# Optimization experiments

Hardware: AMD Instinct MI355X
Metric: run time of the kernel (lower is better)

The kernel has to match this reference:

```python
import jax, jax.numpy as jnp
import numpy as np

N = 1048576        # number of raw proposals
NC = 2             # num classes (source hardcodes self.nc = 2)
CONF_THRES = 0.25  # score_thres
IOU_THRES = 0.45
MAX_WH = 4096.0    # class offset for class-aware NMS (agnostic=False)
MAX_NMS = 30000    # cap on boxes entering NMS
MAX_DET = 300      # cap on detections returned


def setup_inputs() -> dict:
    key = jax.random.key(0)
    k1, k2, k3, k4 = jax.random.split(key, 4)
    xy = jax.random.uniform(k1, (1, N, 2), dtype=jnp.float32) * 640.0          # box centers (pixels)
    wh = jax.random.uniform(k2, (1, N, 2), dtype=jnp.float32) * 98.0 + 2.0     # widths/heights in [2, 100]
    obj = jax.random.uniform(k3, (1, N, 1), dtype=jnp.float32)                 # objectness
    cls = jax.random.uniform(k4, (1, N, NC), dtype=jnp.float32)                # class scores
    prediction = jnp.concatenate([xy, wh, obj, cls], axis=-1)                  # [1, N, 4+1+nc]
    return {"prediction": prediction}


def reference(prediction):
    # Single image (source only ever fills/returns output[0]).
    pred = prediction[0]                        # [N, 7]
    obj = pred[:, 4]                            # objectness
    cls = pred[:, 5:5 + NC] * obj[:, None]      # conf = obj * cls  (nc > 1 branch)
    conf = jnp.max(cls, axis=-1)                # best-class confidence
    j = jnp.argmax(cls, axis=-1)                # best-class index

    # xywh -> xyxy
    xy, wh = pred[:, :2], pred[:, 2:4]
    box = jnp.concatenate([xy - wh * 0.5, xy + wh * 0.5], axis=-1)  # [N, 4]

    # candidate mask: obj > thres (xc) AND best-class conf > thres
    valid = (obj > CONF_THRES) & (conf > CONF_THRES)
    scores = jnp.where(valid, conf, -1.0)

    # n > max_nms: keep top MAX_NMS by confidence (argsort descending truncation)
    top_s, top_i = jax.lax.top_k(scores, MAX_NMS)       # [MAX_NMS]
    box_t = box[top_i]                                   # [MAX_NMS, 4]
    conf_t = conf[top_i]
    j_t = j[top_i]

    # class-aware NMS: offset boxes per class so classes never suppress each other
    boxes_off = box_t + (j_t.astype(box_t.dtype) * MAX_WH)[:, None]
    area = (boxes_off[:, 2] - boxes_off[:, 0]) * (boxes_off[:, 3] - boxes_off[:, 1])

    # Greedy NMS: iteratively select max-score box, suppress IoU > thres.
    # Selecting the argmax each step is equivalent to sorted greedy NMS, and
    # MAX_DET steps yields exactly the first max_det kept indices.
    def step(s, _):
        idx = jnp.argmax(s)
        ok = s[idx] > 0.0                       # any real candidate left?
        b = boxes_off[idx]
        lt = jnp.maximum(b[:2], boxes_off[:, :2])
        rb = jnp.minimum(b[2:], boxes_off[:, 2:])
        inter = jnp.prod(jnp.clip(rb - lt, 0.0), axis=-1)
        iou = inter / (area[idx] + area - inter)
        s = jnp.where(ok & (iou > IOU_THRES), -1.0, s)  # suppress (incl. self, IoU=1)
        return s, (idx, ok)

    _, (sel, ok) = jax.lax.scan(step, top_s, None, length=MAX_DET)

    dets = jnp.concatenate(
        [box_t[sel], conf_t[sel, None], j_t[sel, None].astype(box_t.dtype)], axis=-1
    )                                           # [MAX_DET, 6] = [xyxy, conf, cls]
    dets = dets * ok[:, None].astype(dets.dtype)  # zero out padding rows
    return dets, ok
```

## Files before the change

kernel.cpp:

```cpp
#include <hip/hip_runtime.h>
#include <stdint.h>

#pragma clang fp contract(off)

#define N_ELEM   1048576
#define MAX_NMS  30000
#define MAX_DET  300
#define IOU_T    0.45f
#define CONF_T   0.25f
#define SOA_N    30720
#define KMIN     0xBE800000u
#define EQCAP    2048
#define RPW      16

typedef uint32_t u32;
typedef unsigned long long u64;

#define C_CB   0
#define C_KP   1
#define C_A    2
#define C_NUM  3
#define C_EQC  4

__device__ inline u32 monokey(float s){
  u32 b = __float_as_uint(s);
  return b ^ ((b & 0x80000000u) ? 0xFFFFFFFFu : 0x80000000u);
}
__device__ inline int binOf(u32 k){
  u32 d = (k - KMIN) >> 8;
  return d > 65535u ? 65535 : (int)d;
}
__device__ inline u64 shfl64(u64 v, int src){
  int lo = __shfl((int)(u32)(v & 0xFFFFFFFFull), src);
  int hi = __shfl((int)(u32)(v >> 32), src);
  return ((u64)(u32)hi << 32) | (u32)lo;
}

__global__ void kkeys(const float4* __restrict__ pred4, u32* __restrict__ keys,
                      u32* __restrict__ hist){
  __shared__ float lds[1792];
  int t = threadIdx.x;
  const float4* src = pred4 + (size_t)blockIdx.x * 448;
  float4* l4 = (float4*)lds;
  #pragma unroll
  for (int k = 0; k < 2; k++){
    int idx = k*256 + t;
    if (idx < 448) l4[idx] = src[idx];
  }
  __syncthreads();
  float obj = lds[t*7 + 4], c0 = lds[t*7 + 5], c1 = lds[t*7 + 6];
  float p0 = c0*obj, p1 = c1*obj;
  float conf = fmaxf(p0, p1);
  bool valid = (obj > CONF_T) && (conf > CONF_T);
  float score = valid ? conf : -1.0f;
  u32 mk = monokey(score);
  keys[blockIdx.x*256 + t] = mk;
  if (mk > KMIN) atomicAdd(&hist[binOf(mk)], 1u);
}

__global__ void __launch_bounds__(1024) kselect(const u32* __restrict__ hist,
                                                u32* __restrict__ binBase,
                                                u32* __restrict__ ctrl){
  __shared__ u32 csum[1024];
  __shared__ u32 s[1024];
  __shared__ int selC;
  __shared__ u32 chunk[64];
  int t = threadIdx.x, lane = t & 63, wv = t >> 6;
  for (int j = 0; j < 64; j++){
    int c = wv*64 + j;
    u32 v = hist[c*64 + lane];
    #pragma unroll
    for (int off = 32; off > 0; off >>= 1) v += __shfl_down(v, off);
    if (lane == 0) csum[c] = v;
  }
  __syncthreads();
  u32 own = csum[t];
  s[t] = own; __syncthreads();
  for (int off = 1; off < 1024; off <<= 1){
    u32 v = s[t];
    u32 add = (t + off < 1024) ? s[t + off] : 0u;
    __syncthreads();
    s[t] = v + add;
    __syncthreads();
  }
  u32 above = s[t] - own;
  u32 grand = s[0];
  csum[t] = above;
  const u32 K = MAX_NMS;
  if (grand >= K && above < K && K <= above + own){ selC = t; }
  __syncthreads();
  if (grand >= K && t < 64) chunk[t] = hist[selC*64 + t];
  __syncthreads();
  if (t == 0){
    if (grand < K){
      ctrl[C_CB] = 0xFFFFFFFFu; ctrl[C_KP] = 0; ctrl[C_A] = grand; ctrl[C_NUM] = grand;
    } else {
      u32 cum = csum[selC];
      for (int b = 63; b >= 0; b--){
        u32 c = chunk[b];
        if (cum + c >= K){
          ctrl[C_CB] = (u32)(selC*64 + b);
          ctrl[C_KP] = K - cum;
          ctrl[C_A]  = cum;
          ctrl[C_NUM] = K;
          break;
        }
        cum += c;
      }
    }
  }
  for (int j = 0; j < 64; j++){
    int c = wv*64 + j;
    u32 v = hist[c*64 + lane];
    u32 suf = v;
    #pragma unroll
    for (int off = 1; off < 64; off <<= 1){
      u32 o = __shfl_down(suf, off);
      suf += (lane + off < 64) ? o : 0u;
    }
    binBase[c*64 + lane] = csum[c] + suf - v;
  }
}

__global__ void kscatter(const uint4* __restrict__ keys4, const u32* __restrict__ binBase,
                         u32* __restrict__ binCursor, u32* __restrict__ ctrl,
                         u32* __restrict__ binnedKey, u32* __restrict__ binnedIdx,
                         u32* __restrict__ eqKey, u32* __restrict__ eqIdx){
  int t = blockIdx.x*blockDim.x + threadIdx.x;
  if (t >= N_ELEM/4) return;
  int cb = (int)ctrl[C_CB];
  uint4 kv = keys4[t];
  u32 kk[4] = {kv.x, kv.y, kv.z, kv.w};
  #pragma unroll
  for (int r = 0; r < 4; r++){
    u32 k = kk[r];
    if (k <= KMIN) continue;
    int b = binOf(k);
    u32 i = (u32)(t*4 + r);
    if (b > cb){
      u32 pos = binBase[b] + atomicAdd(&binCursor[b], 1u);
      if (pos < MAX_NMS){ binnedKey[pos] = k; binnedIdx[pos] = i; }
    } else if (b == cb){
      u32 e = atomicAdd(&ctrl[C_EQC], 1u);
      if (e < EQCAP){ eqKey[e] = k; eqIdx[e] = i; }
    }
  }
}

__device__ inline void writeSoA(const float* __restrict__ pred, float* __restrict__ soa,
                                u32 r, u32 i){
  const float* row = pred + (size_t)i*7;
  float x = row[0], y = row[1], w = row[2], hh = row[3];
  float obj = row[4], c0 = row[5], c1 = row[6];
  float p0 = c0*obj, p1 = c1*obj;
  float conf = fmaxf(p0, p1);
  float jf = (p0 >= p1) ? 0.0f : 1.0f;
  float bx1 = x - w*0.5f, by1 = y - hh*0.5f;
  float bx2 = x + w*0.5f, by2 = y + hh*0.5f;
  float off = jf * 4096.0f;
  float ox1 = bx1 + off, oy1 = by1 + off, ox2 = bx2 + off, oy2 = by2 + off;
  float area = (ox2 - ox1) * (oy2 - oy1);
  soa[r + 0*SOA_N] = ox1;  soa[r + 1*SOA_N] = oy1;
  soa[r + 2*SOA_N] = ox2;  soa[r + 3*SOA_N] = oy2;
  soa[r + 4*SOA_N] = area; soa[r + 5*SOA_N] = conf;
  soa[r + 6*SOA_N] = jf;
  soa[r + 7*SOA_N] = bx1;  soa[r + 8*SOA_N] = by1;
  soa[r + 9*SOA_N] = bx2;  soa[r +10*SOA_N] = by2;
}

__global__ void krank(const float* __restrict__ pred, const u32* __restrict__ binnedKey,
                      const u32* __restrict__ binnedIdx, const u32* __restrict__ binBase,
                      const u32* __restrict__ binHist, const u32* __restrict__ ctrl,
                      const u32* __restrict__ eqKey, const u32* __restrict__ eqIdx,
                      float* __restrict__ soa){
  int p = blockIdx.x*blockDim.x + threadIdx.x;
  u32 A = ctrl[C_A], Kp = ctrl[C_KP];
  if (Kp > 0){
    u32 n = ctrl[C_EQC]; if (n > EQCAP) n = EQCAP;
    if (p < (int)n){
      u32 k = eqKey[p], i = eqIdx[p];
      u32 r = 0;
      for (u32 m = 0; m < n; m++){
        u32 km = eqKey[m], im = eqIdx[m];
        r += (km > k) || (km == k && im < i);
      }
      if (r < Kp) writeSoA(pred, soa, A + r, i);
    }
  }
  if (p < (int)A){
    u32 k = binnedKey[p]; u32 i = binnedIdx[p];
    if (i >= N_ELEM) i = 0;
    int b = binOf(k);
    u32 st = binBase[b], cnt = binHist[b];
    u32 r = st;
    for (u32 q = st; q < st + cnt; q++){
      u32 kq = binnedKey[q], iq = binnedIdx[q];
      if (kq > k || (kq == k && iq < i)) r++;
    }
    if (r < A) writeSoA(pred, soa, r, i);
  }
}

__global__ void kmask(const float* __restrict__ soa, u64* __restrict__ mask,
                      int W, int WBsh, int nUnits){
  int lane = threadIdx.x & 63;
  int gw = (blockIdx.x*blockDim.x + threadIdx.x) >> 6;
  int nwaves = (gridDim.x*blockDim.x) >> 6;
  int WB = 1 << WBsh;
  for (int u = gw; u < nUnits; u += nwaves){
    int rowg = u >> WBsh;
    int w = u & (WB - 1);
    if (((w + 1) << 6) <= rowg*RPW) continue;
    int j = (w << 6) + lane;
    float cx1 = soa[j], cy1 = soa[j + SOA_N], cx2 = soa[j + 2*SOA_N],
          cy2 = soa[j + 3*SOA_N], ca = soa[j + 4*SOA_N];
    #pragma unroll
    for (int rr = 0; rr < RPW; rr++){
      int i = rowg*RPW + rr;
      if (w < (i >> 6)) continue;
      float rx1 = soa[i], ry1 = soa[i + SOA_N], rx2 = soa[i + 2*SOA_N],
            ry2 = soa[i + 3*SOA_N], ra = soa[i + 4*SOA_N];
      float ltx = fmaxf(rx1, cx1), lty = fmaxf(ry1, cy1);
      float rbx = fminf(rx2, cx2), rby = fminf(ry2, cy2);
      float iw = fmaxf(rbx - ltx, 0.0f), ih = fmaxf(rby - lty, 0.0f);
      float inter = iw * ih;
      float iou = inter / ((ra + ca) - inter);
      u64 m = __ballot(iou > IOU_T);
      if (lane == 0) mask[(size_t)i*WB + w] = m;
    }
  }
}

__global__ void __launch_bounds__(64) kwalk(const float* __restrict__ soa,
                                            const u64* __restrict__ mask,
                                            const u32* __restrict__ ctrl,
                                            float* __restrict__ out, int out_size,
                                            int W){
  __shared__ float kx1[320], ky1[320], kx2[320], ky2[320], ka[320];
  __shared__ u64 dlds[64];
  int lane = threadIdx.x;
  for (int o = lane; o < out_size; o += 64) out[o] = 0.0f;
  int numCand = (int)ctrl[C_NUM];
  int WB = W >> 6;
  int lim = numCand < W ? numCand : W;
  int nb = (lim + 63) >> 6;
  u64 rem0 = 0, rem1 = 0;
  int nsel = 0;

  u64 diag = 0;
  if (nb > 0 && lane < lim) diag = mask[(size_t)lane*WB + 0];

  for (int bi = 0; bi < nb && nsel < MAX_DET; bi++){
    u64 remw = (bi < 64) ? shfl64(rem0, bi) : shfl64(rem1, bi - 64);
    u64 w = ~remw;
    int rb = lim - (bi << 6);
    if (rb < 64) w &= ((1ull << rb) - 1ull);
    dlds[lane] = diag;
    __syncthreads();

    u64 diagn = 0;
    int inext = (bi + 1)*64 + lane;
    if (bi + 1 < nb && inext < lim) diagn = mask[(size_t)inext*WB + (bi + 1)];

    u64 sel = 0;
    int room = MAX_DET - nsel;
    while (w){
      int b = (int)__builtin_ctzll(w);
      sel |= (1ull << b);
      if (--room == 0) break;
      u64 rw = dlds[b];
      w &= ~rw;
      w &= ~(1ull << b);
    }
    int cnt = __popcll(sel);

    u64 s = sel;
    long long ids[8];
    #pragma unroll
    for (int q = 0; q < 8; q++){
      if (s){ ids[q] = (long long)((bi << 6) + __builtin_ctzll(s)); s &= s - 1; }
      else ids[q] = -1;
    }
    u64 a0[8], a1[8];
    #pragma unroll
    for (int q = 0; q < 8; q++){
      a0[q] = 0; a1[q] = 0;
      if (ids[q] >= 0){
        const u64* rp = mask + (size_t)ids[q]*WB;
        if (lane < WB)      a0[q] = rp[lane];
        if (64 + lane < WB) a1[q] = rp[64 + lane];
      }
    }

    if (lane < cnt){
      u64 t = sel;
      for (int q = 0; q < lane; q++) t &= t - 1;
      int b = (int)__builtin_ctzll(t);
      int i = (bi << 6) + b;
      int r = nsel + lane;
      kx1[r] = soa[i];            ky1[r] = soa[i + SOA_N];
      kx2[r] = soa[i + 2*SOA_N];  ky2[r] = soa[i + 3*SOA_N];
      ka[r]  = soa[i + 4*SOA_N];
      float* dr = out + r*6;
      dr[0] = soa[i + 7*SOA_N];  dr[1] = soa[i + 8*SOA_N];
      dr[2] = soa[i + 9*SOA_N];  dr[3] = soa[i + 10*SOA_N];
      dr[4] = soa[i + 5*SOA_N];  dr[5] = soa[i + 6*SOA_N];
      out[MAX_DET*6 + r] = 1.0f;
    }
    nsel += cnt;

    #pragma unroll
    for (int q = 0; q < 8; q++){ rem0 |= a0[q]; rem1 |= a1[q]; }

    while (s){
      long long ids2[8];
      #pragma unroll
      for (int q = 0; q < 8; q++){
        if (s){ ids2[q] = (long long)((bi << 6) + __builtin_ctzll(s)); s &= s - 1; }
        else ids2[q] = -1;
      }
      u64 b0[8], b1[8];
      #pragma unroll
      for (int q = 0; q < 8; q++){
        b0[q] = 0; b1[q] = 0;
        if (ids2[q] >= 0){
          const u64* rp = mask + (size_t)ids2[q]*WB;
          if (lane < WB)      b0[q] = rp[lane];
          if (64 + lane < WB) b1[q] = rp[64 + lane];
        }
      }
      #pragma unroll
      for (int q = 0; q < 8; q++){ rem0 |= b0[q]; rem1 |= b1[q]; }
    }
    diag = diagn;
    __syncthreads();
  }

  if (nsel < MAX_DET && numCand > W){
    for (int base = W; base < numCand && nsel < MAX_DET; base += 64){
      int li = base + lane;
      bool has = li < numCand;
      float cox1=0.f,coy1=0.f,cox2=0.f,coy2=0.f,car=1.f,csc=-1.f,ccl=0.f;
      float cbx1=0.f,cby1=0.f,cbx2=0.f,cby2=0.f;
      if (has){
        cox1 = soa[li]; coy1 = soa[li + SOA_N]; cox2 = soa[li + 2*SOA_N];
        coy2 = soa[li + 3*SOA_N]; car = soa[li + 4*SOA_N];
        csc = soa[li + 5*SOA_N]; ccl = soa[li + 6*SOA_N];
        cbx1 = soa[li + 7*SOA_N]; cby1 = soa[li + 8*SOA_N];
        cbx2 = soa[li + 9*SOA_N]; cby2 = soa[li + 10*SOA_N];
      }
      int m = min(64, numCand - base);
      for (int t2 = 0; t2 < m && nsel < MAX_DET; t2++){
        float qx1 = __shfl(cox1, t2), qy1 = __shfl(coy1, t2);
        float qx2 = __shfl(cox2, t2), qy2 = __shfl(coy2, t2);
        float qa  = __shfl(car,  t2);
        bool supp = false;
        #pragma unroll
        for (int q = 0; q < 5; q++){
          int slot = lane + (q << 6);
          if (slot < nsel){
            float ltx = fmaxf(qx1, kx1[slot]), lty = fmaxf(qy1, ky1[slot]);
            float rbx = fminf(qx2, kx2[slot]), rby = fminf(qy2, ky2[slot]);
            float iw = fmaxf(rbx - ltx, 0.0f), ih = fmaxf(rby - lty, 0.0f);
            float inter = iw * ih;
            float iou = inter / ((qa + ka[slot]) - inter);
            supp = supp || (iou > IOU_T);
          }
        }
        if (__any(supp)) continue;
        float bx1 = __shfl(cbx1, t2), by1 = __shfl(cby1, t2);
        float bx2 = __shfl(cbx2, t2), by2 = __shfl(cby2, t2);
        float sc  = __shfl(csc,  t2), cl  = __shfl(ccl,  t2);
        if (lane == 0){
          kx1[nsel] = qx1; ky1[nsel] = qy1; kx2[nsel] = qx2; ky2[nsel] = qy2; ka[nsel] = qa;
          float* dr = out + nsel*6;
          dr[0] = bx1; dr[1] = by1; dr[2] = bx2; dr[3] = by2; dr[4] = sc; dr[5] = cl;
          out[MAX_DET*6 + nsel] = 1.0f;
        }
        nsel++;
      }
    }
  }
}

extern "C" void kernel_launch(void* const* d_in, const int* in_sizes, int n_in,
                              void* d_out, int out_size, void* d_ws, size_t ws_size,
                              hipStream_t stream){
  const float* pred = (const float*)d_in[0];
  float* out = (float*)d_out;
  char* w = (char*)d_ws;

  u32*  keys       = (u32*)(w + 0x000000);
  u32*  hist       = (u32*)(w + 0x400000);
  u32*  binCursor  = (u32*)(w + 0x440000);
  u32*  ctrl       = (u32*)(w + 0x480000);
  u32*  binBase    = (u32*)(w + 0x4C0000);
  u32*  eqKey      = (u32*)(w + 0x500000);
  u32*  eqIdx      = (u32*)(w + 0x502000);
  u32*  binnedKey  = (u32*)(w + 0x510000);
  u32*  binnedIdx  = (u32*)(w + 0x530000);
  float* soa       = (float*)(w + 0x550000);
  u64*  mask       = (u64*)(w + 0x6A0000);

  int W, WBsh;
  if      (ws_size >= 0xEA0000){ W = 8192; WBsh = 7; }
  else if (ws_size >= 0x8A0000){ W = 4096; WBsh = 6; }
  else                         { W = 2048; WBsh = 5; }

  hipMemsetAsync(hist, 0, 0x80100, stream);

  kkeys   <<<4096, 256, 0, stream>>>((const float4*)pred, keys, hist);
  kselect <<<1, 1024, 0, stream>>>(hist, binBase, ctrl);
  kscatter<<<1024, 256, 0, stream>>>((const uint4*)keys, binBase, binCursor, ctrl,
                                     binnedKey, binnedIdx, eqKey, eqIdx);
  krank   <<<(MAX_NMS + 255)/256 + 1, 256, 0, stream>>>(pred, binnedKey, binnedIdx, binBase,
                                                        hist, ctrl, eqKey, eqIdx, soa);
  int nUnits = (W/RPW) << WBsh;
  kmask   <<<2048, 256, 0, stream>>>(soa, mask, W, WBsh, nUnits);
  kwalk   <<<1, 64, 0, stream>>>(soa, mask, ctrl, out, out_size, W);
}
```

Before: 325.3 us.

## Fuse selection pipeline into one cooperative kernel with grid syncs

Merges the histogram, threshold selection, scatter, rank and mask-building stages into a single cooperative kernel of 512 blocks separated by grid-wide barriers, replacing five launches plus a memset. The single-block selection step is spread across blocks: each block computes chunk sums in parallel and redundantly does the 256-wide scan. The aim is to remove launch gaps and the serial single-block selection kernel. In exchange, the grid barriers add overhead, and the rank and mask stages now run on a smaller fixed grid with occupancy capped by launch bounds.

```diff
diff --git a/kernel.cpp b/kernel.cpp
--- a/kernel.cpp
+++ b/kernel.cpp
@@ -1,7 +1,10 @@
 #include <hip/hip_runtime.h>
+#include <hip/hip_cooperative_groups.h>
 #include <stdint.h>
 
 #pragma clang fp contract(off)
+
+namespace cg = cooperative_groups;
 
 #define N_ELEM   1048576
 #define MAX_NMS  30000
@@ -12,6 +15,8 @@
 #define KMIN     0xBE800000u
 #define EQCAP    2048
 #define RPW      16
+#define GRID     512
+#define NTHR     (GRID*256)
 
 typedef uint32_t u32;
 typedef unsigned long long u64;
@@ -36,116 +41,13 @@
   return ((u64)(u32)hi << 32) | (u32)lo;
 }
 
-__global__ void kkeys(const float4* __restrict__ pred4, u32* __restrict__ keys,
-                      u32* __restrict__ hist){
-  __shared__ float lds[1792];
-  int t = threadIdx.x;
-  const float4* src = pred4 + (size_t)blockIdx.x * 448;
-  float4* l4 = (float4*)lds;
-  #pragma unroll
-  for (int k = 0; k < 2; k++){
-    int idx = k*256 + t;
-    if (idx < 448) l4[idx] = src[idx];
-  }
-  __syncthreads();
-  float obj = lds[t*7 + 4], c0 = lds[t*7 + 5], c1 = lds[t*7 + 6];
-  float p0 = c0*obj, p1 = c1*obj;
-  float conf = fmaxf(p0, p1);
-  bool valid = (obj > CONF_T) && (conf > CONF_T);
-  float score = valid ? conf : -1.0f;
-  u32 mk = monokey(score);
-  keys[blockIdx.x*256 + t] = mk;
-  if (mk > KMIN) atomicAdd(&hist[binOf(mk)], 1u);
-}
-
-__global__ void __launch_bounds__(1024) kselect(const u32* __restrict__ hist,
-                                                u32* __restrict__ binBase,
-                                                u32* __restrict__ ctrl){
-  __shared__ u32 csum[1024];
-  __shared__ u32 s[1024];
-  __shared__ int selC;
-  __shared__ u32 chunk[64];
-  int t = threadIdx.x, lane = t & 63, wv = t >> 6;
-  for (int j = 0; j < 64; j++){
-    int c = wv*64 + j;
-    u32 v = hist[c*64 + lane];
-    #pragma unroll
-    for (int off = 32; off > 0; off >>= 1) v += __shfl_down(v, off);
-    if (lane == 0) csum[c] = v;
-  }
-  __syncthreads();
-  u32 own = csum[t];
-  s[t] = own; __syncthreads();
-  for (int off = 1; off < 1024; off <<= 1){
-    u32 v = s[t];
-    u32 add = (t + off < 1024) ? s[t + off] : 0u;
-    __syncthreads();
-    s[t] = v + add;
-    __syncthreads();
-  }
-  u32 above = s[t] - own;
-  u32 grand = s[0];
-  csum[t] = above;
-  const u32 K = MAX_NMS;
-  if (grand >= K && above < K && K <= above + own){ selC = t; }
-  __syncthreads();
-  if (grand >= K && t < 64) chunk[t] = hist[selC*64 + t];
-  __syncthreads();
-  if (t == 0){
-    if (grand < K){
-      ctrl[C_CB] = 0xFFFFFFFFu; ctrl[C_KP] = 0; ctrl[C_A] = grand; ctrl[C_NUM] = grand;
-    } else {
-      u32 cum = csum[selC];
-      for (int b = 63; b >= 0; b--){
-        u32 c = chunk[b];
-        if (cum + c >= K){
-          ctrl[C_CB] = (u32)(selC*64 + b);
-          ctrl[C_KP] = K - cum;
-          ctrl[C_A]  = cum;
-          ctrl[C_NUM] = K;
-          break;
-        }
-        cum += c;
-      }
-    }
-  }
-  for (int j = 0; j < 64; j++){
-    int c = wv*64 + j;
-    u32 v = hist[c*64 + lane];
-    u32 suf = v;
-    #pragma unroll
-    for (int off = 1; off < 64; off <<= 1){
-      u32 o = __shfl_down(suf, off);
-      suf += (lane + off < 64) ? o : 0u;
-    }
-    binBase[c*64 + lane] = csum[c] + suf - v;
-  }
-}
-
-__global__ void kscatter(const uint4* __restrict__ keys4, const u32* __restrict__ binBase,
-                         u32* __restrict__ binCursor, u32* __restrict__ ctrl,
-                         u32* __restrict__ binnedKey, u32* __restrict__ binnedIdx,
-                         u32* __restrict__ eqKey, u32* __restrict__ eqIdx){
-  int t = blockIdx.x*blockDim.x + threadIdx.x;
-  if (t >= N_ELEM/4) return;
-  int cb = (int)ctrl[C_CB];
-  uint4 kv = keys4[t];
-  u32 kk[4] = {kv.x, kv.y, kv.z, kv.w};
-  #pragma unroll
-  for (int r = 0; r < 4; r++){
-    u32 k = kk[r];
-    if (k <= KMIN) continue;
-    int b = binOf(k);
-    u32 i = (u32)(t*4 + r);
-    if (b > cb){
-      u32 pos = binBase[b] + atomicAdd(&binCursor[b], 1u);
-      if (pos < MAX_NMS){ binnedKey[pos] = k; binnedIdx[pos] = i; }
-    } else if (b == cb){
-      u32 e = atomicAdd(&ctrl[C_EQC], 1u);
-      if (e < EQCAP){ eqKey[e] = k; eqIdx[e] = i; }
-    }
-  }
-}
+struct KParams {
+  const float* pred;
+  u32* keys; u32* hist; u32* binCursor; u32* ctrl; u32* chunkSum;
+  u32* binBase; u32* eqKey; u32* eqIdx; u32* binnedKey; u32* binnedIdx;
+  float* soa; u64* mask;
+  int W, WBsh;
+};
 
 __device__ inline void writeSoA(const float* __restrict__ pred, float* __restrict__ soa,
                                 u32 r, u32 i){
@@ -168,65 +70,208 @@
   soa[r + 9*SOA_N] = bx2;  soa[r +10*SOA_N] = by2;
 }
 
-__global__ void krank(const float* __restrict__ pred, const u32* __restrict__ binnedKey,
-                      const u32* __restrict__ binnedIdx, const u32* __restrict__ binBase,
-                      const u32* __restrict__ binHist, const u32* __restrict__ ctrl,
-                      const u32* __restrict__ eqKey, const u32* __restrict__ eqIdx,
-                      float* __restrict__ soa){
-  int p = blockIdx.x*blockDim.x + threadIdx.x;
-  u32 A = ctrl[C_A], Kp = ctrl[C_KP];
-  if (Kp > 0){
-    u32 n = ctrl[C_EQC]; if (n > EQCAP) n = EQCAP;
-    if (p < (int)n){
-      u32 k = eqKey[p], i = eqIdx[p];
-      u32 r = 0;
-      for (u32 m = 0; m < n; m++){
-        u32 km = eqKey[m], im = eqIdx[m];
-        r += (km > k) || (km == k && im < i);
-      }
-      if (r < Kp) writeSoA(pred, soa, A + r, i);
-    }
-  }
-  if (p < (int)A){
-    u32 k = binnedKey[p]; u32 i = binnedIdx[p];
-    if (i >= N_ELEM) i = 0;
-    int b = binOf(k);
-    u32 st = binBase[b], cnt = binHist[b];
-    u32 r = st;
-    for (u32 q = st; q < st + cnt; q++){
-      u32 kq = binnedKey[q], iq = binnedIdx[q];
-      if (kq > k || (kq == k && iq < i)) r++;
-    }
-    if (r < A) writeSoA(pred, soa, r, i);
-  }
-}
-
-__global__ void kmask(const float* __restrict__ soa, u64* __restrict__ mask,
-                      int W, int WBsh, int nUnits){
-  int lane = threadIdx.x & 63;
-  int gw = (blockIdx.x*blockDim.x + threadIdx.x) >> 6;
-  int nwaves = (gridDim.x*blockDim.x) >> 6;
-  int WB = 1 << WBsh;
-  for (int u = gw; u < nUnits; u += nwaves){
-    int rowg = u >> WBsh;
-    int w = u & (WB - 1);
-    if (((w + 1) << 6) <= rowg*RPW) continue;
-    int j = (w << 6) + lane;
-    float cx1 = soa[j], cy1 = soa[j + SOA_N], cx2 = soa[j + 2*SOA_N],
-          cy2 = soa[j + 3*SOA_N], ca = soa[j + 4*SOA_N];
+__global__ void __launch_bounds__(256, 2) kfused(KParams P){
+  cg::grid_group grid = cg::this_grid();
+  int tid = threadIdx.x, bid = blockIdx.x;
+  int gtid = bid*256 + tid;
+  int lane = tid & 63, wv = tid >> 6;
+
+  __shared__ float stage[1792];
+  __shared__ u32 csum[1024];
+  __shared__ u32 s256[256];
+  __shared__ u32 above[1024];
+  __shared__ int selC;
+  __shared__ u32 dl[64];
+
+  if (gtid < 65536){ P.hist[gtid] = 0; P.binCursor[gtid] = 0; }
+  if (gtid < 64) P.ctrl[gtid] = 0;
+  grid.sync();
+
+  {
+    const float4* pred4 = (const float4*)P.pred;
+    for (int tile = 0; tile < 8; tile++){
+      int tb = bid*8 + tile;
+      const float4* src = pred4 + (size_t)tb*448;
+      float4* l4 = (float4*)stage;
+      __syncthreads();
+      #pragma unroll
+      for (int k = 0; k < 2; k++){
+        int idx = k*256 + tid;
+        if (idx < 448) l4[idx] = src[idx];
+      }
+      __syncthreads();
+      float obj = stage[tid*7+4], c0 = stage[tid*7+5], c1 = stage[tid*7+6];
+      float p0 = c0*obj, p1 = c1*obj;
+      float conf = fmaxf(p0, p1);
+      bool valid = (obj > CONF_T) && (conf > CONF_T);
+      float score = valid ? conf : -1.0f;
+      u32 mk = monokey(score);
+      P.keys[tb*256 + tid] = mk;
+      if (mk > KMIN) atomicAdd(&P.hist[binOf(mk)], 1u);
+    }
+  }
+  grid.sync();
+
+  if (wv < 2){
+    int c = bid*2 + wv;
+    u32 v = P.hist[c*64 + lane];
     #pragma unroll
-    for (int rr = 0; rr < RPW; rr++){
-      int i = rowg*RPW + rr;
-      if (w < (i >> 6)) continue;
-      float rx1 = soa[i], ry1 = soa[i + SOA_N], rx2 = soa[i + 2*SOA_N],
-            ry2 = soa[i + 3*SOA_N], ra = soa[i + 4*SOA_N];
-      float ltx = fmaxf(rx1, cx1), lty = fmaxf(ry1, cy1);
-      float rbx = fminf(rx2, cx2), rby = fminf(ry2, cy2);
-      float iw = fmaxf(rbx - ltx, 0.0f), ih = fmaxf(rby - lty, 0.0f);
-      float inter = iw * ih;
-      float iou = inter / ((ra + ca) - inter);
-      u64 m = __ballot(iou > IOU_T);
-      if (lane == 0) mask[(size_t)i*WB + w] = m;
+    for (int off = 32; off > 0; off >>= 1) v += __shfl_down(v, off);
+    if (lane == 0) P.chunkSum[c] = v;
+  }
+  grid.sync();
+
+  {
+    for (int j = 0; j < 4; j++) csum[j*256 + tid] = P.chunkSum[j*256 + tid];
+    __syncthreads();
+    u32 o0 = csum[tid*4], o1 = csum[tid*4+1], o2 = csum[tid*4+2], o3 = csum[tid*4+3];
+    u32 g = o0 + o1 + o2 + o3;
+    s256[tid] = g; __syncthreads();
+    for (int off = 1; off < 256; off <<= 1){
+      u32 v = s256[tid];
+      u32 add = (tid + off < 256) ? s256[tid + off] : 0u;
+      __syncthreads();
+      s256[tid] = v + add;
+      __syncthreads();
+    }
+    u32 aboveG = s256[tid] - g;
+    u32 grand = s256[0];
+    above[tid*4+0] = aboveG + o1 + o2 + o3;
+    above[tid*4+1] = aboveG + o2 + o3;
+    above[tid*4+2] = aboveG + o3;
+    above[tid*4+3] = aboveG;
+    const u32 K = MAX_NMS;
+    if (tid == 0) selC = 0;
+    __syncthreads();
+    #pragma unroll
+    for (int j = 0; j < 4; j++){
+      int c = tid*4 + j;
+      u32 ab = above[c], cs = csum[c];
+      if (grand >= K && ab < K && K <= ab + cs) selC = c;
+    }
+    __syncthreads();
+    if (bid == 0){
+      if (grand < K){
+        if (tid == 0){
+          P.ctrl[C_CB] = 0xFFFFFFFFu; P.ctrl[C_KP] = 0;
+          P.ctrl[C_A] = grand; P.ctrl[C_NUM] = grand;
+        }
+      } else {
+        if (tid < 64) dl[tid] = P.hist[selC*64 + tid];
+        __syncthreads();
+        if (tid == 0){
+          u32 cum = above[selC];
+          for (int b = 63; b >= 0; b--){
+            u32 c = dl[b];
+            if (cum + c >= K){
+              P.ctrl[C_CB] = (u32)(selC*64 + b);
+              P.ctrl[C_KP] = K - cum;
+              P.ctrl[C_A]  = cum;
+              P.ctrl[C_NUM] = K;
+              break;
+            }
+            cum += c;
+          }
+        }
+      }
+    }
+    __syncthreads();
+    if (wv < 2){
+      int c = bid*2 + wv;
+      u32 v = P.hist[c*64 + lane];
+      u32 suf = v;
+      #pragma unroll
+      for (int off = 1; off < 64; off <<= 1){
+        u32 o = __shfl_down(suf, off);
+        suf += (lane + off < 64) ? o : 0u;
+      }
+      P.binBase[c*64 + lane] = above[c] + suf - v;
+    }
+  }
+  grid.sync();
+
+  {
+    const uint4* keys4 = (const uint4*)P.keys;
+    int cb = (int)P.ctrl[C_CB];
+    for (int t4 = gtid; t4 < N_ELEM/4; t4 += NTHR){
+      uint4 kv = keys4[t4];
+      u32 kk[4] = {kv.x, kv.y, kv.z, kv.w};
+      #pragma unroll
+      for (int r = 0; r < 4; r++){
+        u32 k = kk[r];
+        if (k <= KMIN) continue;
+        int b = binOf(k);
+        u32 i = (u32)(t4*4 + r);
+        if (b > cb){
+          u32 pos = P.binBase[b] + atomicAdd(&P.binCursor[b], 1u);
+          if (pos < MAX_NMS){ P.binnedKey[pos] = k; P.binnedIdx[pos] = i; }
+        } else if (b == cb){
+          u32 e = atomicAdd(&P.ctrl[C_EQC], 1u);
+          if (e < EQCAP){ P.eqKey[e] = k; P.eqIdx[e] = i; }
+        }
+      }
+    }
+  }
+  grid.sync();
+
+  {
+    int p = gtid;
+    u32 A = P.ctrl[C_A], Kp = P.ctrl[C_KP];
+    if (Kp > 0){
+      u32 n = P.ctrl[C_EQC]; if (n > EQCAP) n = EQCAP;
+      if (p < (int)n){
+        u32 k = P.eqKey[p], i = P.eqIdx[p];
+        u32 r = 0;
+        for (u32 m = 0; m < n; m++){
+          u32 km = P.eqKey[m], im = P.eqIdx[m];
+          r += (km > k) || (km == k && im < i);
+        }
+        if (r < Kp) writeSoA(P.pred, P.soa, A + r, i);
+      }
+    }
+    if (p < (int)A){
+      u32 k = P.binnedKey[p]; u32 i = P.binnedIdx[p];
+      if (i >= N_ELEM) i = 0;
+      int b = binOf(k);
+      u32 st = P.binBase[b], cnt = P.hist[b];
+      u32 r = st;
+      for (u32 q = st; q < st + cnt; q++){
+        u32 kq = P.binnedKey[q], iq = P.binnedIdx[q];
+        if (kq > k || (kq == k && iq < i)) r++;
+      }
+      if (r < A) writeSoA(P.pred, P.soa, r, i);
+    }
+  }
+  grid.sync();
+
+  {
+    const float* soa = P.soa;
+    u64* mask = P.mask;
+    int gw = gtid >> 6;
+    int nwaves = NTHR >> 6;
+    int WB = 1 << P.WBsh;
+    int nUnits = (P.W/RPW) << P.WBsh;
+    for (int u = gw; u < nUnits; u += nwaves){
+      int rowg = u >> P.WBsh;
+      int w = u & (WB - 1);
+      if (((w + 1) << 6) <= rowg*RPW) continue;
+      int j = (w << 6) + lane;
+      float cx1 = soa[j], cy1 = soa[j + SOA_N], cx2 = soa[j + 2*SOA_N],
+            cy2 = soa[j + 3*SOA_N], ca = soa[j + 4*SOA_N];
+      #pragma unroll
+      for (int rr = 0; rr < RPW; rr++){
+        int i = rowg*RPW + rr;
+        if (w < (i >> 6)) continue;
+        float rx1 = soa[i], ry1 = soa[i + SOA_N], rx2 = soa[i + 2*SOA_N],
+              ry2 = soa[i + 3*SOA_N], ra = soa[i + 4*SOA_N];
+        float ltx = fmaxf(rx1, cx1), lty = fmaxf(ry1, cy1);
+        float rbx = fminf(rx2, cx2), rby = fminf(ry2, cy2);
+        float iw = fmaxf(rbx - ltx, 0.0f), ih = fmaxf(rby - lty, 0.0f);
+        float inter = iw * ih;
+        float iou = inter / ((ra + ca) - inter);
+        u64 m = __ballot(iou > IOU_T);
+        if (lane == 0) mask[(size_t)i*WB + w] = m;
+      }
     }
   }
 }
@@ -390,32 +435,26 @@
   float* out = (float*)d_out;
   char* w = (char*)d_ws;
 
-  u32*  keys       = (u32*)(w + 0x000000);
-  u32*  hist       = (u32*)(w + 0x400000);
-  u32*  binCursor  = (u32*)(w + 0x440000);
-  u32*  ctrl       = (u32*)(w + 0x480000);
-  u32*  binBase    = (u32*)(w + 0x4C0000);
-  u32*  eqKey      = (u32*)(w + 0x500000);
-  u32*  eqIdx      = (u32*)(w + 0x502000);
-  u32*  binnedKey  = (u32*)(w + 0x510000);
-  u32*  binnedIdx  = (u32*)(w + 0x530000);
-  float* soa       = (float*)(w + 0x550000);
-  u64*  mask       = (u64*)(w + 0x6A0000);
-
-  int W, WBsh;
-  if      (ws_size >= 0xEA0000){ W = 8192; WBsh = 7; }
-  else if (ws_size >= 0x8A0000){ W = 4096; WBsh = 6; }
-  else                         { W = 2048; WBsh = 5; }
-
-  hipMemsetAsync(hist, 0, 0x80100, stream);
-
-  kkeys   <<<4096, 256, 0, stream>>>((const float4*)pred, keys, hist);
-  kselect <<<1, 1024, 0, stream>>>(hist, binBase, ctrl);
-  kscatter<<<1024, 256, 0, stream>>>((const uint4*)keys, binBase, binCursor, ctrl,
-                                     binnedKey, binnedIdx, eqKey, eqIdx);
-  krank   <<<(MAX_NMS + 255)/256 + 1, 256, 0, stream>>>(pred, binnedKey, binnedIdx, binBase,
-                                                        hist, ctrl, eqKey, eqIdx, soa);
-  int nUnits = (W/RPW) << WBsh;
-  kmask   <<<2048, 256, 0, stream>>>(soa, mask, W, WBsh, nUnits);
-  kwalk   <<<1, 64, 0, stream>>>(soa, mask, ctrl, out, out_size, W);
-}
+  KParams P;
+  P.pred      = pred;
+  P.keys      = (u32*)(w + 0x000000);
+  P.hist      = (u32*)(w + 0x400000);
+  P.binCursor = (u32*)(w + 0x440000);
+  P.ctrl      = (u32*)(w + 0x480000);
+  P.chunkSum  = (u32*)(w + 0x484000);
+  P.binBase   = (u32*)(w + 0x4C0000);
+  P.eqKey     = (u32*)(w + 0x500000);
+  P.eqIdx     = (u32*)(w + 0x502000);
+  P.binnedKey = (u32*)(w + 0x510000);
+  P.binnedIdx = (u32*)(w + 0x530000);
+  P.soa       = (float*)(w + 0x550000);
+  P.mask      = (u64*)(w + 0x6A0000);
+
+  if      (ws_size >= 0xEA0000){ P.W = 8192; P.WBsh = 7; }
+  else if (ws_size >= 0x8A0000){ P.W = 4096; P.WBsh = 6; }
+  else                         { P.W = 2048; P.WBsh = 5; }
+
+  void* args[] = { (void*)&P };
+  hipLaunchCooperativeKernel((const void*)kfused, dim3(GRID), dim3(256), args, 0, stream);
+  kwalk<<<1, 64, 0, stream>>>(P.soa, P.mask, P.ctrl, out, out_size, P.W);
+}
```

After: 672.0 us. 107% more time.
